# Performance work log

Measured on AMD Instinct MI355X. Metric: run time of the kernel, lower is better.

## Reference

```python
import jax, jax.numpy as jnp
import numpy as np

B, C, N = 8, 512, 2048

def setup_inputs() -> dict:
    key = jax.random.key(0)
    ks = jax.random.split(key, 7)
    s = 1.0 / np.sqrt(C)
    return {
        "x": jax.random.normal(ks[0], (B, C, N), dtype=jnp.float32),
        "wq": jax.random.normal(ks[1], (C, C), dtype=jnp.float32) * s,
        "bq": jax.random.normal(ks[2], (C,), dtype=jnp.float32) * s,
        "wk": jax.random.normal(ks[3], (C, C), dtype=jnp.float32) * s,
        "bk": jax.random.normal(ks[4], (C,), dtype=jnp.float32) * s,
        "wv": jax.random.normal(ks[5], (C, C), dtype=jnp.float32) * s,
        "bv": jax.random.normal(ks[6], (C,), dtype=jnp.float32) * s,
    }

def reference(x, wq, bq, wk, bk, wv, bv):
    # Conv1d with kernel=1 == pointwise channel matmul: [B,C,N] -> [B,C,N]
    q = jnp.einsum('oc,bcn->bon', wq, x) + bq[None, :, None]
    k = jnp.einsum('oc,bcn->bon', wk, x) + bk[None, :, None]
    v = jnp.einsum('oc,bcn->bon', wv, x) + bv[None, :, None]
    # scores[b,i,j] = sum_c q[b,c,i] * k[b,c,j]; softmax over j (no scaling, as in source)
    scores = jnp.einsum('bci,bcj->bij', q, k)
    attn = jax.nn.softmax(scores, axis=-1)  # [B,N,N]
    # out[b,c,i] = sum_j v[b,c,j] * attn[b,i,j]
    out = jnp.einsum('bcj,bij->bci', v, attn)
    return out + x
```

## Files before the change

### kernel.cpp

```cpp
#include <hip/hip_runtime.h>
#include <hip/hip_bf16.h>

typedef _Float16 half_t;
typedef _Float16 f16x8 __attribute__((ext_vector_type(8)));
typedef float f32x4 __attribute__((ext_vector_type(4)));

#define AS1 __attribute__((address_space(1)))
#define AS3 __attribute__((address_space(3)))

constexpr int CB = 512;
constexpr int NB = 2048;
constexpr int BB = 8;

__device__ inline f32x4 mfma16(f16x8 a, f16x8 b, f32x4 c) {
  return __builtin_amdgcn_mfma_f32_16x16x32_f16(a, b, c, 0, 0, 0);
}

__device__ inline void xcd_swizzle(int& bx, int& by, int& bz) {
  const int gx = gridDim.x, gy = gridDim.y, gz = gridDim.z;
  const int nwg = gx * gy * gz;
  int lin = blockIdx.x + gx * (blockIdx.y + gy * blockIdx.z);
  if ((nwg & 7) == 0) {
    const int q = nwg >> 3;
    lin = (lin & 7) * q + (lin >> 3);
  }
  bx = lin % gx;
  int tmp = lin / gx;
  by = tmp % gy;
  bz = tmp / gy;
}

__global__ void convert_w(const float* __restrict__ wv, half_t* __restrict__ wvh) {
  int i = blockIdx.x * 256 + threadIdx.x;
  if (i < CB * CB) wvh[i] = (half_t)wv[i];
}

__global__ __launch_bounds__(256) void compute_G_part(const float* __restrict__ wq,
                                                      const float* __restrict__ wk,
                                                      float* __restrict__ Gp) {
  __shared__ float aq[64][68];
  __shared__ float ak[64][68];
  const int c0 = blockIdx.y * 64, d0 = blockIdx.x * 64, o0 = blockIdx.z * 64;
  const int t = threadIdx.x;
  {
    const int r = t >> 2, cbase = (t & 3) * 16;
    const float* q = wq + (size_t)(o0 + r) * CB + c0 + cbase;
    const float* k = wk + (size_t)(o0 + r) * CB + d0 + cbase;
#pragma unroll
    for (int q4 = 0; q4 < 4; q4++) {
      *(float4*)&aq[r][cbase + q4 * 4] = *(const float4*)(q + q4 * 4);
      *(float4*)&ak[r][cbase + q4 * 4] = *(const float4*)(k + q4 * 4);
    }
  }
  __syncthreads();
  const int tc = t & 15, td = t >> 4;
  float acc[4][4] = {};
#pragma unroll 8
  for (int o = 0; o < 64; o++) {
    float4 a4 = *(const float4*)&aq[o][tc * 4];
    float4 b4 = *(const float4*)&ak[o][td * 4];
    float av[4] = {a4.x, a4.y, a4.z, a4.w};
    float bv[4] = {b4.x, b4.y, b4.z, b4.w};
#pragma unroll
    for (int i = 0; i < 4; i++)
#pragma unroll
      for (int j = 0; j < 4; j++)
        acc[i][j] += av[i] * bv[j];
  }
  float* gz = Gp + (size_t)blockIdx.z * CB * CB;
#pragma unroll
  for (int i = 0; i < 4; i++) {
    int c = c0 + tc * 4 + i;
#pragma unroll
    for (int j = 0; j < 4; j++)
      gz[(size_t)c * CB + d0 + td * 4 + j] = acc[i][j];
  }
}

__global__ void reduce_G(const float* __restrict__ Gp, half_t* __restrict__ Gh) {
  int i = blockIdx.x * 256 + threadIdx.x;
  if (i >= CB * CB) return;
  float s = 0.0f;
#pragma unroll
  for (int z = 0; z < 8; z++) s += Gp[(size_t)z * CB * CB + i];
  Gh[i] = (half_t)s;
}

__global__ void compute_u(const float* __restrict__ wk, const float* __restrict__ bq,
                          float* __restrict__ u) {
  int d = blockIdx.x * 256 + threadIdx.x;
  if (d >= CB) return;
  float s = 0.0f;
  for (int o = 0; o < CB; o++) s += bq[o] * wk[(size_t)o * CB + d];
  u[d] = s;
}

__global__ __launch_bounds__(256) void compute_ubias(const half_t* __restrict__ xh,
                                                     const float* __restrict__ u,
                                                     float* __restrict__ ub) {
  __shared__ float us[CB];
  for (int i = threadIdx.x; i < CB; i += 256) us[i] = u[i];
  __syncthreads();
  int row = blockIdx.x * 4 + (threadIdx.x >> 6);
  int lane = threadIdx.x & 63;
  f16x8 vh = *(const f16x8*)(xh + (size_t)row * CB + lane * 8);
  float s = 0.0f;
#pragma unroll
  for (int i = 0; i < 8; i++) s += us[lane * 8 + i] * (float)vh[i];
#pragma unroll
  for (int off = 32; off; off >>= 1) s += __shfl_xor(s, off);
  if (lane == 0) ub[row] = s;
}

__global__ void transpose_x(const float* __restrict__ x, half_t* __restrict__ oh,
                            half_t* __restrict__ xn) {
  __shared__ float tile[32][33];
  int b = blockIdx.z, c0 = blockIdx.y * 32, n0 = blockIdx.x * 32;
  int tx = threadIdx.x, ty = threadIdx.y;
  const float* xb = x + (size_t)b * CB * NB;
  half_t* xnb = xn + (size_t)b * CB * NB;
#pragma unroll
  for (int r = 0; r < 4; r++) {
    float v = xb[(size_t)(c0 + ty + 8 * r) * NB + n0 + tx];
    tile[ty + 8 * r][tx] = v;
    xnb[(size_t)(c0 + ty + 8 * r) * NB + n0 + tx] = (half_t)v;
  }
  __syncthreads();
  size_t base = (size_t)b * NB * CB;
#pragma unroll
  for (int r = 0; r < 4; r++)
    oh[base + (size_t)(n0 + ty + 8 * r) * CB + c0 + tx] = (half_t)tile[tx][ty + 8 * r];
}

template <int BIAS, int EPI>
__global__ __launch_bounds__(256) void gemm_nt(
    const half_t* __restrict__ A, int lda, long sA,
    const half_t* __restrict__ Bh, int ldb, long sB,
    void* __restrict__ D, int ldd, long sD,
    const float* __restrict__ bias, long sBias,
    const half_t* __restrict__ R, int ldr, long sR,
    int K) {
  constexpr int TSZ = 128 * 32;
  __shared__ alignas(16) half_t sm[2 * 2 * TSZ];

  int bxi, byi, bzi;
  xcd_swizzle(bxi, byi, bzi);
  const int t = threadIdx.x;
  const int z = bzi;
  const half_t* Ab  = A  + (size_t)z * sA + (size_t)(byi * 128) * lda;
  const half_t* Bbh = Bh + (size_t)z * sB + (size_t)(bxi * 128) * ldb;
  const int wid = t >> 6, l15 = t & 15, hi = (t >> 4) & 3;
  const int wr = wid >> 1, wc = wid & 1;
  const int lineA = t >> 2, eoff = (t & 3) * 8;

  f32x4 acc[4][4] = {};

  auto stage = [&](int buf, int kt) {
    half_t* base = sm + buf * (2 * TSZ);
#pragma unroll
    for (int p = 0; p < 2; p++) {
      size_t goA = (size_t)(p * 64 + lineA) * lda + kt * 32 + eoff;
      size_t goB = (size_t)(p * 64 + lineA) * ldb + kt * 32 + eoff;
      int lo = p * 2048 + t * 8;
      __builtin_amdgcn_global_load_lds((const AS1 void*)(Ab + goA),  (AS3 void*)(base + lo), 16, 0, 0);
      __builtin_amdgcn_global_load_lds((const AS1 void*)(Bbh + goB), (AS3 void*)(base + TSZ + lo), 16, 0, 0);
    }
  };

  const int nt = K >> 5;
  stage(0, 0);
  __syncthreads();
  int cur = 0;
  for (int kt = 0; kt < nt; kt++) {
    if (kt + 1 < nt) stage(cur ^ 1, kt + 1);
    const half_t* bb = sm + cur * (2 * TSZ);
    f16x8 af[4], bfh[4];
#pragma unroll
    for (int f = 0; f < 4; f++) {
      af[f]  = *(const f16x8*)(bb + (wr * 64 + f * 16 + l15) * 32 + hi * 8);
      bfh[f] = *(const f16x8*)(bb + TSZ + (wc * 64 + f * 16 + l15) * 32 + hi * 8);
    }
#pragma unroll
    for (int fm = 0; fm < 4; fm++)
#pragma unroll
      for (int fn = 0; fn < 4; fn++)
        acc[fm][fn] = mfma16(af[fm], bfh[fn], acc[fm][fn]);
    __syncthreads();
    cur ^= 1;
  }

  const int row0 = byi * 128 + wr * 64;
  const int col0 = bxi * 128 + wc * 64;
#pragma unroll
  for (int fm = 0; fm < 4; fm++) {
    int rowb = row0 + fm * 16 + hi * 4;
#pragma unroll
    for (int fn = 0; fn < 4; fn++) {
      int col = col0 + fn * 16 + l15;
      float bc = (BIAS == 1) ? bias[(size_t)z * sBias + col] : 0.0f;
#pragma unroll
      for (int r = 0; r < 4; r++) {
        float val = acc[fm][fn][r] + bc;
        size_t di = (size_t)(rowb + r) * ldd + col;
        if (EPI == 3) {
          val += (float)R[(size_t)z * sR + (size_t)(rowb + r) * ldr + col];
          ((float*)D)[(size_t)z * sD + di] = val;
        } else {
          float sv = fminf(fmaxf(val * 256.0f, -32767.0f), 32767.0f);
          ((short*)D)[(size_t)z * sD + di] = (short)__float2int_rn(sv);
        }
      }
    }
  }
}

__global__ __launch_bounds__(256) void gemm_vyt(
    const half_t* __restrict__ xh, const half_t* __restrict__ wvh,
    const half_t* __restrict__ Gh, const float* __restrict__ bv,
    half_t* __restrict__ v, half_t* __restrict__ YTh) {
  constexpr int TSZ = 128 * 32;
  __shared__ alignas(16) half_t sm[2 * 2 * TSZ];

  int bxi, byi, bzi;
  xcd_swizzle(bxi, byi, bzi);
  const int t = threadIdx.x;

  const half_t* Ab;
  const half_t* Bb;
  half_t* Dz;
  int ldd, row0b, col0b;
  const float* rowbias = nullptr;
  if (bzi < 8) {
    const int z = bzi;
    Ab = wvh + (size_t)(byi * 128) * CB;
    Bb = xh + (size_t)z * NB * CB + (size_t)(bxi * 128) * CB;
    Dz = v + (size_t)z * CB * NB;
    ldd = NB; row0b = byi * 128; col0b = bxi * 128;
    rowbias = bv;
  } else {
    const int z = bzi - 8;
    const int lin2 = byi * 16 + bxi;
    const int xp = lin2 & 3, yp = lin2 >> 2;
    Ab = xh + (size_t)z * NB * CB + (size_t)(yp * 128) * CB;
    Bb = Gh + (size_t)(xp * 128) * CB;
    Dz = YTh + (size_t)z * NB * CB;
    ldd = CB; row0b = yp * 128; col0b = xp * 128;
  }

  const int wid = t >> 6, l15 = t & 15, hi = (t >> 4) & 3;
  const int wr = wid >> 1, wc = wid & 1;
  const int lineA = t >> 2, eoff = (t & 3) * 8;

  f32x4 acc[4][4] = {};

  auto stage = [&](int buf, int kt) {
    half_t* base = sm + buf * (2 * TSZ);
#pragma unroll
    for (int p = 0; p < 2; p++) {
      size_t go = (size_t)(p * 64 + lineA) * CB + kt * 32 + eoff;
      int lo = p * 2048 + t * 8;
      __builtin_amdgcn_global_load_lds((const AS1 void*)(Ab + go), (AS3 void*)(base + lo), 16, 0, 0);
      __builtin_amdgcn_global_load_lds((const AS1 void*)(Bb + go), (AS3 void*)(base + TSZ + lo), 16, 0, 0);
    }
  };

  stage(0, 0);
  __syncthreads();
  int cur = 0;
  for (int kt = 0; kt < 16; kt++) {
    if (kt + 1 < 16) stage(cur ^ 1, kt + 1);
    const half_t* bb = sm + cur * (2 * TSZ);
    f16x8 af[4], bf[4];
#pragma unroll
    for (int f = 0; f < 4; f++) {
      af[f] = *(const f16x8*)(bb + (wr * 64 + f * 16 + l15) * 32 + hi * 8);
      bf[f] = *(const f16x8*)(bb + TSZ + (wc * 64 + f * 16 + l15) * 32 + hi * 8);
    }
#pragma unroll
    for (int fm = 0; fm < 4; fm++)
#pragma unroll
      for (int fn = 0; fn < 4; fn++)
        acc[fm][fn] = mfma16(af[fm], bf[fn], acc[fm][fn]);
    __syncthreads();
    cur ^= 1;
  }

  const int row0 = row0b + wr * 64;
  const int col0 = col0b + wc * 64;
#pragma unroll
  for (int fm = 0; fm < 4; fm++) {
    int rowb = row0 + fm * 16 + hi * 4;
#pragma unroll
    for (int fn = 0; fn < 4; fn++) {
      int col = col0 + fn * 16 + l15;
#pragma unroll
      for (int r = 0; r < 4; r++) {
        float val = acc[fm][fn][r];
        if (rowbias) val += rowbias[rowb + r];
        Dz[(size_t)(rowb + r) * ldd + col] = (half_t)val;
      }
    }
  }
}

struct alignas(16) H8 { half_t h[8]; };
struct alignas(16) S8 { short s[8]; };

__global__ __launch_bounds__(256) void softmax_rows(const short* __restrict__ S,
                                                    half_t* __restrict__ P) {
  const short* row = S + (size_t)blockIdx.x * NB;
  int t = threadIdx.x;
  S8 r8 = *reinterpret_cast<const S8*>(row + t * 8);
  float vals[8];
#pragma unroll
  for (int i = 0; i < 8; i++) vals[i] = (float)r8.s[i] * 0.00390625f;
  float m = vals[0];
#pragma unroll
  for (int i = 1; i < 8; i++) m = fmaxf(m, vals[i]);
#pragma unroll
  for (int off = 32; off; off >>= 1) m = fmaxf(m, __shfl_xor(m, off));
  __shared__ float redm[4], reds[4];
  if ((t & 63) == 0) redm[t >> 6] = m;
  __syncthreads();
  m = fmaxf(fmaxf(redm[0], redm[1]), fmaxf(redm[2], redm[3]));
  float e[8], s = 0.0f;
#pragma unroll
  for (int i = 0; i < 8; i++) { e[i] = __expf(vals[i] - m); s += e[i]; }
#pragma unroll
  for (int off = 32; off; off >>= 1) s += __shfl_xor(s, off);
  if ((t & 63) == 0) reds[t >> 6] = s;
  __syncthreads();
  s = reds[0] + reds[1] + reds[2] + reds[3];
  float inv = 1.0f / s;
  H8 ob;
#pragma unroll
  for (int i = 0; i < 8; i++) ob.h[i] = (half_t)(e[i] * inv);
  *reinterpret_cast<H8*>(P + (size_t)blockIdx.x * NB + t * 8) = ob;
}

extern "C" void kernel_launch(void* const* d_in, const int* in_sizes, int n_in,
                              void* d_out, int out_size, void* d_ws, size_t ws_size,
                              hipStream_t stream) {
  const float* x  = (const float*)d_in[0];
  const float* wq = (const float*)d_in[1];
  const float* bq = (const float*)d_in[2];
  const float* wk = (const float*)d_in[3];
  const float* wv = (const float*)d_in[5];
  const float* bv = (const float*)d_in[6];
  float* out = (float*)d_out;

  const size_t MB = 1u << 20;
  if (ws_size < 196 * MB) return;

  char* ws = (char*)d_ws;
  half_t* xh   = (half_t*)(ws + 0);
  half_t* YTh  = (half_t*)(ws + 16 * MB);
  half_t* v    = (half_t*)(ws + 32 * MB);
  short*  Ss   = (short*)(ws + 48 * MB);
  float*  Gp   = (float*)(ws + 48 * MB);
  half_t* Pd   = (half_t*)(ws + 112 * MB);
  half_t* xn   = (half_t*)(ws + 176 * MB);
  half_t* Gh   = (half_t*)(ws + 192 * MB);
  half_t* wvh  = (half_t*)(ws + 192 * MB + 512 * 1024);
  float*  u    = (float*)(ws + 193 * MB);
  float*  ub   = (float*)(ws + 193 * MB + 256 * 1024);

  convert_w<<<1024, 256, 0, stream>>>(wv, wvh);
  compute_G_part<<<dim3(8, 8, 8), 256, 0, stream>>>(wq, wk, Gp);
  reduce_G<<<1024, 256, 0, stream>>>(Gp, Gh);
  compute_u<<<2, 256, 0, stream>>>(wk, bq, u);
  transpose_x<<<dim3(64, 16, 8), dim3(32, 8), 0, stream>>>(x, xh, xn);
  compute_ubias<<<BB * NB / 4, 256, 0, stream>>>(xh, u, ub);

  gemm_vyt<<<dim3(16, 4, 16), 256, 0, stream>>>(xh, wvh, Gh, bv, v, YTh);

  gemm_nt<1, 4><<<dim3(16, 16, 8), 256, 0, stream>>>(
      xh, CB, (long)NB * CB,
      YTh, CB, (long)NB * CB,
      Ss, NB, (long)NB * NB, ub, NB, nullptr, 0, 0, CB);

  softmax_rows<<<BB * NB, 256, 0, stream>>>(Ss, Pd);

  gemm_nt<0, 3><<<dim3(16, 4, 8), 256, 0, stream>>>(
      v, NB, (long)CB * NB,
      Pd, NB, (long)NB * NB,
      out, NB, (long)CB * NB, nullptr, 0,
      xn, NB, (long)CB * NB, NB);
}
```

Before: 203.1 us.

## Triple-buffer GEMM LDS pipeline with vmcnt waits and merge prep kernels

```diff
diff --git a/kernel.cpp b/kernel.cpp
--- a/kernel.cpp
+++ b/kernel.cpp
@@ -30,9 +30,20 @@
   bz = tmp / gy;
 }
 
-__global__ void convert_w(const float* __restrict__ wv, half_t* __restrict__ wvh) {
-  int i = blockIdx.x * 256 + threadIdx.x;
-  if (i < CB * CB) wvh[i] = (half_t)wv[i];
+__global__ void prep_wu(const float* __restrict__ wv, const float* __restrict__ wk,
+                        const float* __restrict__ bq,
+                        half_t* __restrict__ wvh, float* __restrict__ u) {
+  if (blockIdx.x < 1024) {
+    int i = blockIdx.x * 256 + threadIdx.x;
+    if (i < CB * CB) wvh[i] = (half_t)wv[i];
+  } else {
+    int d = (blockIdx.x - 1024) * 256 + threadIdx.x;
+    if (d < CB) {
+      float s = 0.0f;
+      for (int o = 0; o < CB; o++) s += bq[o] * wk[(size_t)o * CB + d];
+      u[d] = s;
+    }
+  }
 }
 
 __global__ __launch_bounds__(256) void compute_G_part(const float* __restrict__ wq,
@@ -86,15 +97,6 @@
   Gh[i] = (half_t)s;
 }
 
-__global__ void compute_u(const float* __restrict__ wk, const float* __restrict__ bq,
-                          float* __restrict__ u) {
-  int d = blockIdx.x * 256 + threadIdx.x;
-  if (d >= CB) return;
-  float s = 0.0f;
-  for (int o = 0; o < CB; o++) s += bq[o] * wk[(size_t)o * CB + d];
-  u[d] = s;
-}
-
 __global__ __launch_bounds__(256) void compute_ubias(const half_t* __restrict__ xh,
                                                      const float* __restrict__ u,
                                                      float* __restrict__ ub) {
@@ -132,16 +134,15 @@
     oh[base + (size_t)(n0 + ty + 8 * r) * CB + c0 + tx] = (half_t)tile[tx][ty + 8 * r];
 }
 
-template <int BIAS, int EPI>
+template <int BIAS, int EPI, int NT>
 __global__ __launch_bounds__(256) void gemm_nt(
     const half_t* __restrict__ A, int lda, long sA,
     const half_t* __restrict__ Bh, int ldb, long sB,
     void* __restrict__ D, int ldd, long sD,
     const float* __restrict__ bias, long sBias,
-    const half_t* __restrict__ R, int ldr, long sR,
-    int K) {
+    const half_t* __restrict__ R, int ldr, long sR) {
   constexpr int TSZ = 128 * 32;
-  __shared__ alignas(16) half_t sm[2 * 2 * TSZ];
+  __shared__ alignas(16) half_t sm[3 * 2 * TSZ];
 
   int bxi, byi, bzi;
   xcd_swizzle(bxi, byi, bzi);
@@ -167,26 +168,38 @@
     }
   };
 
-  const int nt = K >> 5;
   stage(0, 0);
-  __syncthreads();
-  int cur = 0;
-  for (int kt = 0; kt < nt; kt++) {
-    if (kt + 1 < nt) stage(cur ^ 1, kt + 1);
-    const half_t* bb = sm + cur * (2 * TSZ);
-    f16x8 af[4], bfh[4];
+  stage(1, 1);
+  asm volatile("s_waitcnt vmcnt(4)" ::: "memory");
+  __builtin_amdgcn_s_barrier();
+  asm volatile("" ::: "memory");
+
+  int rb = 0;
+  for (int kt = 0; kt < NT; kt++) {
+    if (kt + 2 < NT) {
+      int sb = rb + 2; if (sb >= 3) sb -= 3;
+      stage(sb, kt + 2);
+    }
+    const half_t* bb = sm + rb * (2 * TSZ);
+    f16x8 af[4], bf[4];
 #pragma unroll
     for (int f = 0; f < 4; f++) {
-      af[f]  = *(const f16x8*)(bb + (wr * 64 + f * 16 + l15) * 32 + hi * 8);
-      bfh[f] = *(const f16x8*)(bb + TSZ + (wc * 64 + f * 16 + l15) * 32 + hi * 8);
+      af[f] = *(const f16x8*)(bb + (wr * 64 + f * 16 + l15) * 32 + hi * 8);
+      bf[f] = *(const f16x8*)(bb + TSZ + (wc * 64 + f * 16 + l15) * 32 + hi * 8);
     }
 #pragma unroll
     for (int fm = 0; fm < 4; fm++)
 #pragma unroll
       for (int fn = 0; fn < 4; fn++)
-        acc[fm][fn] = mfma16(af[fm], bfh[fn], acc[fm][fn]);
-    __syncthreads();
-    cur ^= 1;
+        acc[fm][fn] = mfma16(af[fm], bf[fn], acc[fm][fn]);
+
+    if (kt + 1 < NT) {
+      if (kt + 2 < NT) asm volatile("s_waitcnt vmcnt(4)" ::: "memory");
+      else             asm volatile("s_waitcnt vmcnt(0)" ::: "memory");
+      __builtin_amdgcn_s_barrier();
+      asm volatile("" ::: "memory");
+    }
+    rb = (rb + 1 == 3) ? 0 : rb + 1;
   }
 
   const int row0 = byi * 128 + wr * 64;
@@ -365,25 +378,24 @@
   float*  u    = (float*)(ws + 193 * MB);
   float*  ub   = (float*)(ws + 193 * MB + 256 * 1024);
 
-  convert_w<<<1024, 256, 0, stream>>>(wv, wvh);
+  prep_wu<<<1026, 256, 0, stream>>>(wv, wk, bq, wvh, u);
   compute_G_part<<<dim3(8, 8, 8), 256, 0, stream>>>(wq, wk, Gp);
   reduce_G<<<1024, 256, 0, stream>>>(Gp, Gh);
-  compute_u<<<2, 256, 0, stream>>>(wk, bq, u);
   transpose_x<<<dim3(64, 16, 8), dim3(32, 8), 0, stream>>>(x, xh, xn);
   compute_ubias<<<BB * NB / 4, 256, 0, stream>>>(xh, u, ub);
 
   gemm_vyt<<<dim3(16, 4, 16), 256, 0, stream>>>(xh, wvh, Gh, bv, v, YTh);
 
-  gemm_nt<1, 4><<<dim3(16, 16, 8), 256, 0, stream>>>(
+  gemm_nt<1, 4, 16><<<dim3(16, 16, 8), 256, 0, stream>>>(
       xh, CB, (long)NB * CB,
       YTh, CB, (long)NB * CB,
-      Ss, NB, (long)NB * NB, ub, NB, nullptr, 0, 0, CB);
+      Ss, NB, (long)NB * NB, ub, NB, nullptr, 0, 0);
 
   softmax_rows<<<BB * NB, 256, 0, stream>>>(Ss, Pd);
 
-  gemm_nt<0, 3><<<dim3(16, 4, 8), 256, 0, stream>>>(
+  gemm_nt<0, 3, 64><<<dim3(16, 4, 8), 256, 0, stream>>>(
       v, NB, (long)CB * NB,
       Pd, NB, (long)NB * NB,
       out, NB, (long)CB * NB, nullptr, 0,
-      xn, NB, (long)CB * NB, NB);
-}
+      xn, NB, (long)CB * NB);
+}
```

New measurement: 209.5 us. 1.03x slower.
